# Optimization experiments

Measured on AMD Instinct MI355X. Metric: run time of the kernel, lower is better.

The kernel has to match this reference:

```python
import jax, jax.numpy as jnp
import numpy as np

NUM_BINS = 256

def setup_inputs() -> dict:
    key = jax.random.key(0)
    k1, k2 = jax.random.split(key)
    B, C, H, W = 32, 3, 512, 512
    # images in [-1, 1], matching the torch module's denorm x*0.5+0.5
    imgs = jax.random.uniform(k1, (B, C, H, W), dtype=jnp.float32) * 2.0 - 1.0
    target_hist = jax.random.uniform(k2, (B, NUM_BINS), dtype=jnp.float32)
    return {"generated_img_batch": imgs, "target_hist_batch": target_hist}


def _batch_histograms(images, num_bins):
    # images: [B, C, H, W] in [-1, 1]
    B = images.shape[0]
    denorm = images * 0.5 + 0.5                       # [0, 1]
    idx = (denorm * (num_bins - 1)).astype(jnp.int32)  # [B, C, H, W]
    idx = idx.reshape(B, -1)                           # [B, C*H*W]
    rows = jnp.arange(B, dtype=jnp.int32)[:, None]
    hist = jnp.zeros((B, num_bins), dtype=jnp.float32)
    hist = hist.at[rows, idx].add(1.0)
    return hist


def reference(generated_img_batch, target_hist_batch):
    eps = 1e-8
    gen_hist = _batch_histograms(generated_img_batch, NUM_BINS)
    gen_p = gen_hist / (gen_hist.sum(axis=1, keepdims=True) + eps)
    tgt_p = target_hist_batch / (target_hist_batch.sum(axis=1, keepdims=True) + eps)
    gen_cdf = jnp.cumsum(gen_p, axis=1)
    tgt_cdf = jnp.cumsum(tgt_p, axis=1)
    return jnp.mean(jnp.abs(gen_cdf - tgt_cdf))
```

## Files before the change

kernel.cpp:

```cpp
#include <hip/hip_runtime.h>

#define NUM_BINS 256
#define BATCH 32
#define CHW (3 * 512 * 512)
#define N4 (CHW / 4)
#define BPB 64

#define GH_ELEMS (BATCH * BPB * NUM_BINS)

__global__ __launch_bounds__(256) void hist_kernel(
    const float* __restrict__ img, unsigned int* __restrict__ gh,
    unsigned int* __restrict__ counter) {
  __shared__ unsigned int lh[4][NUM_BINS];
  const int tid  = threadIdx.x;
  const int wave = tid >> 6;
  const int blk  = blockIdx.x;
  const int b    = blockIdx.y;

  if (blk == 0 && b == 0 && tid == 0) *counter = 0u;

  for (int i = tid; i < 4 * NUM_BINS; i += 256)
    ((unsigned int*)lh)[i] = 0u;
  __syncthreads();

  const float4* src = (const float4*)(img + (size_t)b * CHW);
  int i = blk * 256 + tid;
#pragma unroll 4
  for (int it = 0; it < N4 / (BPB * 256); ++it, i += BPB * 256) {
    float4 v = src[i];
    int i0 = (int)((v.x * 0.5f + 0.5f) * 255.0f);
    int i1 = (int)((v.y * 0.5f + 0.5f) * 255.0f);
    int i2 = (int)((v.z * 0.5f + 0.5f) * 255.0f);
    int i3 = (int)((v.w * 0.5f + 0.5f) * 255.0f);
    i0 = min(max(i0, 0), NUM_BINS - 1);
    i1 = min(max(i1, 0), NUM_BINS - 1);
    i2 = min(max(i2, 0), NUM_BINS - 1);
    i3 = min(max(i3, 0), NUM_BINS - 1);
    atomicAdd(&lh[wave][i0], 1u);
    atomicAdd(&lh[wave][i1], 1u);
    atomicAdd(&lh[wave][i2], 1u);
    atomicAdd(&lh[wave][i3], 1u);
  }
  __syncthreads();

  unsigned int s = lh[0][tid] + lh[1][tid] + lh[2][tid] + lh[3][tid];
  gh[((size_t)b * BPB + blk) * NUM_BINS + tid] = s;
}

__global__ __launch_bounds__(256) void loss_kernel(
    const unsigned int* __restrict__ gh, const float* __restrict__ tgt,
    float* __restrict__ partial, unsigned int* __restrict__ counter,
    float* __restrict__ out) {
  __shared__ float2 wsum[4];
  __shared__ float wtot[4];
  __shared__ float wabs[4];
  __shared__ int last_flag;
  const int b = blockIdx.x, tid = threadIdx.x;
  const int lane = tid & 63, wave = tid >> 6;

  float g = 0.0f;
  const unsigned int* gb = gh + (size_t)b * BPB * NUM_BINS + tid;
#pragma unroll 8
  for (int k = 0; k < BPB; ++k) g += (float)gb[k * NUM_BINS];
  float t = tgt[b * NUM_BINS + tid];

  float sg = g, st = t;
#pragma unroll
  for (int off = 32; off > 0; off >>= 1) {
    sg += __shfl_down(sg, off);
    st += __shfl_down(st, off);
  }
  if (lane == 0) wsum[wave] = make_float2(sg, st);
  __syncthreads();
  float sgT = wsum[0].x + wsum[1].x + wsum[2].x + wsum[3].x;
  float stT = wsum[0].y + wsum[1].y + wsum[2].y + wsum[3].y;

  float v = g / (sgT + 1e-8f) - t / (stT + 1e-8f);

  float sv = v;
#pragma unroll
  for (int off = 1; off < 64; off <<= 1) {
    float n = __shfl_up(sv, off);
    if (lane >= off) sv += n;
  }
  if (lane == 63) wtot[wave] = sv;
  __syncthreads();
  float prefix = 0.0f;
  for (int w = 0; w < wave; ++w) prefix += wtot[w];
  sv += prefix;

  float a = fabsf(sv);
#pragma unroll
  for (int off = 32; off > 0; off >>= 1) a += __shfl_down(a, off);
  if (lane == 0) wabs[wave] = a;
  __syncthreads();

  if (tid == 0) {
    float tot = wabs[0] + wabs[1] + wabs[2] + wabs[3];
    atomicExch(&partial[b], tot);
    __threadfence();
    unsigned int old = atomicAdd(counter, 1u);
    last_flag = (old == BATCH - 1) ? 1 : 0;
  }
  __syncthreads();

  if (last_flag && wave == 0) {
    float pv = (lane < BATCH) ? atomicAdd(&partial[lane], 0.0f) : 0.0f;
#pragma unroll
    for (int off = 32; off > 0; off >>= 1) pv += __shfl_down(pv, off);
    if (lane == 0) out[0] = pv / (float)(BATCH * NUM_BINS);
  }
}

extern "C" void kernel_launch(void* const* d_in, const int* in_sizes, int n_in,
                              void* d_out, int out_size, void* d_ws, size_t ws_size,
                              hipStream_t stream) {
  const float* img = (const float*)d_in[0];
  const float* tgt = (const float*)d_in[1];
  float* out = (float*)d_out;

  unsigned int* gh = (unsigned int*)d_ws;
  float* partial = (float*)((char*)d_ws + GH_ELEMS * sizeof(unsigned int));
  unsigned int* counter = (unsigned int*)(partial + BATCH);

  dim3 hgrid(BPB, BATCH, 1);
  hist_kernel<<<hgrid, 256, 0, stream>>>(img, gh, counter);
  loss_kernel<<<BATCH, 256, 0, stream>>>(gh, tgt, partial, counter, out);
}
```

Before: 149.5 us.

## Fuse histogram and loss kernels via global atomics and last-block reduction

Merges the two kernels into one. Each block atomically adds its local histogram into a per-batch global histogram, and the last block to finish each batch computes that batch's CDF loss term. A tiny init kernel zeroes the counters and histograms. The loop is also fully unrolled. This is meant to remove the per-block partial-histogram writes and reads and the separate loss pass, at the cost of an extra launch plus global atomic contention and thread fences.

```diff
diff --git a/kernel.cpp b/kernel.cpp
--- a/kernel.cpp
+++ b/kernel.cpp
@@ -5,19 +5,27 @@
 #define CHW (3 * 512 * 512)
 #define N4 (CHW / 4)
 #define BPB 64
+#define ITERS (N4 / (BPB * 256))
 
-#define GH_ELEMS (BATCH * BPB * NUM_BINS)
+#define HIST_U   (BATCH * NUM_BINS)
+#define INIT_U   (HIST_U + BATCH + 1)
 
-__global__ __launch_bounds__(256) void hist_kernel(
-    const float* __restrict__ img, unsigned int* __restrict__ gh,
-    unsigned int* __restrict__ counter) {
+__global__ __launch_bounds__(256) void init_kernel(unsigned int* __restrict__ ws) {
+  for (int i = threadIdx.x; i < INIT_U; i += 256) ws[i] = 0u;
+}
+
+__global__ __launch_bounds__(256) void fused_kernel(
+    const float* __restrict__ img, const float* __restrict__ tgt,
+    unsigned int* __restrict__ hist, unsigned int* __restrict__ batch_done,
+    unsigned int* __restrict__ all_done, float* __restrict__ partial,
+    float* __restrict__ out) {
   __shared__ unsigned int lh[4][NUM_BINS];
+  __shared__ int last_flag;
   const int tid  = threadIdx.x;
+  const int lane = tid & 63;
   const int wave = tid >> 6;
   const int blk  = blockIdx.x;
   const int b    = blockIdx.y;
-
-  if (blk == 0 && b == 0 && tid == 0) *counter = 0u;
 
   for (int i = tid; i < 4 * NUM_BINS; i += 256)
     ((unsigned int*)lh)[i] = 0u;
@@ -25,8 +33,8 @@
 
   const float4* src = (const float4*)(img + (size_t)b * CHW);
   int i = blk * 256 + tid;
-#pragma unroll 4
-  for (int it = 0; it < N4 / (BPB * 256); ++it, i += BPB * 256) {
+#pragma unroll
+  for (int it = 0; it < ITERS; ++it, i += BPB * 256) {
     float4 v = src[i];
     int i0 = (int)((v.x * 0.5f + 0.5f) * 255.0f);
     int i1 = (int)((v.y * 0.5f + 0.5f) * 255.0f);
@@ -44,25 +52,24 @@
   __syncthreads();
 
   unsigned int s = lh[0][tid] + lh[1][tid] + lh[2][tid] + lh[3][tid];
-  gh[((size_t)b * BPB + blk) * NUM_BINS + tid] = s;
-}
+  atomicAdd(&hist[b * NUM_BINS + tid], s);
+  __threadfence();
+  __syncthreads();
 
-__global__ __launch_bounds__(256) void loss_kernel(
-    const unsigned int* __restrict__ gh, const float* __restrict__ tgt,
-    float* __restrict__ partial, unsigned int* __restrict__ counter,
-    float* __restrict__ out) {
+  if (tid == 0) {
+    unsigned int old = atomicAdd(&batch_done[b], 1u);
+    last_flag = (old == BPB - 1) ? 1 : 0;
+  }
+  __syncthreads();
+  if (!last_flag) return;
+
+  __threadfence();
+  float g = (float)atomicAdd(&hist[b * NUM_BINS + tid], 0u);
+  float t = tgt[b * NUM_BINS + tid];
+
   __shared__ float2 wsum[4];
   __shared__ float wtot[4];
   __shared__ float wabs[4];
-  __shared__ int last_flag;
-  const int b = blockIdx.x, tid = threadIdx.x;
-  const int lane = tid & 63, wave = tid >> 6;
-
-  float g = 0.0f;
-  const unsigned int* gb = gh + (size_t)b * BPB * NUM_BINS + tid;
-#pragma unroll 8
-  for (int k = 0; k < BPB; ++k) g += (float)gb[k * NUM_BINS];
-  float t = tgt[b * NUM_BINS + tid];
 
   float sg = g, st = t;
 #pragma unroll
@@ -99,12 +106,13 @@
     float tot = wabs[0] + wabs[1] + wabs[2] + wabs[3];
     atomicExch(&partial[b], tot);
     __threadfence();
-    unsigned int old = atomicAdd(counter, 1u);
+    unsigned int old = atomicAdd(all_done, 1u);
     last_flag = (old == BATCH - 1) ? 1 : 0;
   }
   __syncthreads();
+  if (!last_flag) return;
 
-  if (last_flag && wave == 0) {
+  if (wave == 0) {
     float pv = (lane < BATCH) ? atomicAdd(&partial[lane], 0.0f) : 0.0f;
 #pragma unroll
     for (int off = 32; off > 0; off >>= 1) pv += __shfl_down(pv, off);
@@ -119,11 +127,14 @@
   const float* tgt = (const float*)d_in[1];
   float* out = (float*)d_out;
 
-  unsigned int* gh = (unsigned int*)d_ws;
-  float* partial = (float*)((char*)d_ws + GH_ELEMS * sizeof(unsigned int));
-  unsigned int* counter = (unsigned int*)(partial + BATCH);
+  unsigned int* ws = (unsigned int*)d_ws;
+  unsigned int* hist = ws;
+  unsigned int* batch_done = ws + HIST_U;
+  unsigned int* all_done = ws + HIST_U + BATCH;
+  float* partial = (float*)(ws + INIT_U);
 
-  dim3 hgrid(BPB, BATCH, 1);
-  hist_kernel<<<hgrid, 256, 0, stream>>>(img, gh, counter);
-  loss_kernel<<<BATCH, 256, 0, stream>>>(gh, tgt, partial, counter, out);
+  init_kernel<<<1, 256, 0, stream>>>(ws);
+  dim3 grid(BPB, BATCH, 1);
+  fused_kernel<<<grid, 256, 0, stream>>>(img, tgt, hist, batch_done, all_done,
+                                         partial, out);
 }
```

New measurement: 325.7 us. 2.18x slower.
